# Kernel tuning notes

Hardware: AMD Instinct MI355X
Metric: run time of the kernel (lower is better)

Reference implementation:

```python
import jax, jax.numpy as jnp
import numpy as np


def setup_inputs() -> dict:
    key = jax.random.key(0)
    k1, k2 = jax.random.split(key)
    B, T, D, E = 4, 4096, 2048, 64
    x = jax.random.normal(k1, (B, T, D), dtype=jnp.float32)
    gate_w = jax.random.normal(k2, (E, D), dtype=jnp.float32) * (1.0 / np.sqrt(D))
    return {"x": x, "gate_w": gate_w, "top_k": 2}


def reference(x, gate_w, top_k):
    B, T, D = x.shape
    x_flat = x.reshape(-1, D)                      # (B*T, D)
    logits = jnp.einsum('nd,ed->ne', x_flat, gate_w)  # (B*T, E)
    weights, indices = jax.lax.top_k(logits, top_k)   # (B*T, K)
    weights = jax.nn.softmax(weights, axis=-1)
    return indices, weights
```

## Files before the change

### kernel.cpp

```cpp
#include <hip/hip_runtime.h>
#include <hip/hip_bf16.h>
#include <math.h>


constexpr int D_DIM = 2048;
constexpr int E_DIM = 64;
constexpr int BM    = 32;
constexpr int BKC   = 64;
constexpr int NCH   = D_DIM / BKC;
constexpr int LPAD  = 68;

typedef __attribute__((ext_vector_type(8))) short s16x8;
typedef __attribute__((ext_vector_type(4))) float f32x4;

static __device__ __forceinline__ short f2bf(float f) {
    __hip_bfloat16 h = __float2bfloat16(f);
    return *reinterpret_cast<short*>(&h);
}
static __device__ __forceinline__ float b2f(short s) {
    union { unsigned u; float f; } x;
    x.u = ((unsigned)(unsigned short)s) << 16;
    return x.f;
}

template <int N> static __device__ __forceinline__ void waitvm() {
    asm volatile("s_waitcnt vmcnt(%0)" :: "n"(N) : "memory");
}

__global__ __launch_bounds__(256, 1)
void pack_w(const float* __restrict__ w, short* __restrict__ wsb) {
    const int idx = blockIdx.x * 256 + threadIdx.x;
    const int e = idx >> 11, k = idx & 2047;
    const float v = w[idx];
    const short hi = f2bf(v);
    const short lo = f2bf(v - b2f(hi));
    const int g = k >> 3, j = k & 7;
    const size_t base = (size_t)g * 1024 + e * 8 + j;
    wsb[base]       = hi;
    wsb[base + 512] = lo;
}

template <bool PACKED>
__global__ __launch_bounds__(512, 4)
void router_v8(const float* __restrict__ x,
               const float* __restrict__ w,
               const short* __restrict__ wsb,
               float* __restrict__ out,
               int nrows) {
    __shared__ alignas(16) float smem[4][BM * BKC / 4 * 4];

    const int t    = threadIdx.x;
    const int lane = t & 63;
    const int wv   = t >> 6;
    const int row0 = blockIdx.x * BM;
    const int l15  = lane & 15;
    const int k8   = lane >> 4;
    const int rsel = wv & 1;
    const int e0w  = (wv >> 1) * 16;
    const int ph   = blockIdx.x & (NCH - 1);
    const char* wsb_b = (const char*)wsb;

    s16x8 Bh[4][2], Bl[4][2];

    auto loadB = [&](int p, int c) {
        const int cc = (c + ph) & (NCH - 1);
        if constexpr (PACKED) {
            #pragma unroll
            for (int s = 0; s < 2; ++s) {
                const char* bp = wsb_b + (size_t)cc * 16384
                               + (s * 4 + k8) * 2048 + (e0w + l15) * 16;
                Bh[p][s] = *reinterpret_cast<const s16x8*>(bp);
                Bl[p][s] = *reinterpret_cast<const s16x8*>(bp + 1024);
            }
        } else {
            #pragma unroll
            for (int s = 0; s < 2; ++s) {
                const float* pw = w + (size_t)(e0w + l15) * D_DIM
                                + cc * BKC + (s * 4 + k8) * 8;
                const float4 w0 = *reinterpret_cast<const float4*>(pw);
                const float4 w1 = *reinterpret_cast<const float4*>(pw + 4);
                const float wvv[8] = {w0.x, w0.y, w0.z, w0.w, w1.x, w1.y, w1.z, w1.w};
                #pragma unroll
                for (int j = 0; j < 8; ++j) {
                    const short h = f2bf(wvv[j]);
                    Bh[p][s][j] = h;
                    Bl[p][s][j] = f2bf(wvv[j] - b2f(h));
                }
            }
        }
    };

    auto stageA = [&](int p, int c) {
        const int cc = (c + ph) & (NCH - 1);
        const int r  = 4 * wv + (lane >> 4);
        const char* src = (const char*)x + (size_t)(row0 + r) * (D_DIM * 4)
                        + cc * 256 + ((l15 * 16) ^ ((r & 7) << 4));
        __builtin_amdgcn_global_load_lds(
            (const __attribute__((address_space(1))) void*)src,
            (__attribute__((address_space(3))) void*)((char*)&smem[p][0] + wv * 1024),
            16, 0, 0);
    };

    f32x4 acc;
    #pragma unroll
    for (int j = 0; j < 4; ++j) acc[j] = 0.f;

    auto compute = [&](int p) {
        const char* rp  = (const char*)&smem[p][0] + (16 * rsel + l15) * 256;
        const int   swz = ((16 * rsel + l15) & 7) << 4;
        #pragma unroll
        for (int s = 0; s < 2; ++s) {
            const int off = s * 128 + k8 * 32;
            const float4 v0 = *reinterpret_cast<const float4*>(rp + (off ^ swz));
            const float4 v1 = *reinterpret_cast<const float4*>(rp + ((off + 16) ^ swz));
            const float vv[8] = {v0.x, v0.y, v0.z, v0.w, v1.x, v1.y, v1.z, v1.w};
            s16x8 ah, al;
            #pragma unroll
            for (int j = 0; j < 8; ++j) {
                const short h = f2bf(vv[j]);
                ah[j] = h;
                al[j] = f2bf(vv[j] - b2f(h));
            }
            acc = __builtin_amdgcn_mfma_f32_16x16x32_bf16(al, Bh[p][s], acc, 0, 0, 0);
            acc = __builtin_amdgcn_mfma_f32_16x16x32_bf16(ah, Bl[p][s], acc, 0, 0, 0);
            acc = __builtin_amdgcn_mfma_f32_16x16x32_bf16(ah, Bh[p][s], acc, 0, 0, 0);
        }
    };

    #pragma unroll
    for (int p = 0; p < 4; ++p) { loadB(p, p); stageA(p, p); }

    #pragma unroll 1
    for (int cq = 0; cq < 7; ++cq) {
        #pragma unroll
        for (int p = 0; p < 4; ++p) {
            waitvm<15>();
            __builtin_amdgcn_s_barrier();
            asm volatile("" ::: "memory");
            compute(p);
            asm volatile("s_waitcnt lgkmcnt(0)" ::: "memory");
            __builtin_amdgcn_s_barrier();
            asm volatile("" ::: "memory");
            const int c = cq * 4 + p + 4;
            loadB(p, c);
            stageA(p, c);
        }
    }
    waitvm<15>(); __builtin_amdgcn_s_barrier(); asm volatile("" ::: "memory"); compute(0);
    waitvm<10>(); __builtin_amdgcn_s_barrier(); asm volatile("" ::: "memory"); compute(1);
    waitvm<5>();  __builtin_amdgcn_s_barrier(); asm volatile("" ::: "memory"); compute(2);
    waitvm<0>();  __builtin_amdgcn_s_barrier(); asm volatile("" ::: "memory"); compute(3);
    __syncthreads();

    float* lgs = &smem[0][0];
    #pragma unroll
    for (int j = 0; j < 4; ++j)
        lgs[(16 * rsel + k8 * 4 + j) * LPAD + e0w + l15] = acc[j];
    __syncthreads();

    if (wv < 4) {
        const int row = wv * 8 + (lane >> 3);
        const int seg = lane & 7;
        const float* rp = &lgs[row * LPAD + seg * 8];
        const float4 a  = *reinterpret_cast<const float4*>(rp);
        const float4 bq = *reinterpret_cast<const float4*>(rp + 4);
        const float sv[8] = {a.x, a.y, a.z, a.w, bq.x, bq.y, bq.z, bq.w};
        float m1 = sv[0]; int i1 = seg * 8;
        float m2 = -INFINITY; int i2 = 0;
        #pragma unroll
        for (int j = 1; j < 8; ++j) {
            const float v = sv[j]; const int idx = seg * 8 + j;
            if (v > m1)      { m2 = m1; i2 = i1; m1 = v; i1 = idx; }
            else if (v > m2) { m2 = v;  i2 = idx; }
        }
        #pragma unroll
        for (int d = 1; d < 8; d <<= 1) {
            const float M1 = __shfl_xor(m1, d); const int I1 = __shfl_xor(i1, d);
            const float M2 = __shfl_xor(m2, d); const int I2 = __shfl_xor(i2, d);
            const bool sw = (M1 > m1) || (M1 == m1 && I1 < i1);
            const float a1 = sw ? M1 : m1; const int j1 = sw ? I1 : i1;
            const float b1 = sw ? m1 : M1; const int kx = sw ? i1 : I1;
            const float a2 = sw ? M2 : m2; const int j2 = sw ? I2 : i2;
            const bool t2 = (b1 > a2) || (b1 == a2 && kx < j2);
            m1 = a1; i1 = j1;
            m2 = t2 ? b1 : a2; i2 = t2 ? kx : j2;
        }
        if (seg == 0) {
            const float e2v = expf(m2 - m1);
            const float sm  = 1.0f + e2v;
            const long  r   = row0 + row;
            const long  off = (long)nrows * 2;
            out[2 * r + 0]       = (float)i1;
            out[2 * r + 1]       = (float)i2;
            out[off + 2 * r + 0] = 1.0f / sm;
            out[off + 2 * r + 1] = e2v / sm;
        }
    }
}

extern "C" void kernel_launch(void* const* d_in, const int* in_sizes, int n_in,
                              void* d_out, int out_size, void* d_ws, size_t ws_size,
                              hipStream_t stream) {
    const float* x = (const float*)d_in[0];
    const float* w = (const float*)d_in[1];
    float* out = (float*)d_out;
    short* wsb = (short*)d_ws;
    const int nrows = in_sizes[0] / D_DIM;
    const int grid  = nrows / BM;
    const bool packed = ws_size >= (size_t)(E_DIM * D_DIM) * 2 * sizeof(short);

    if (packed) {
        hipLaunchKernelGGL(pack_w, dim3(E_DIM * D_DIM / 256), dim3(256), 0, stream, w, wsb);
        hipLaunchKernelGGL(router_v8<true>, dim3(grid), dim3(512), 0, stream,
                           x, w, wsb, out, nrows);
    } else {
        hipLaunchKernelGGL(router_v8<false>, dim3(grid), dim3(512), 0, stream,
                           x, w, wsb, out, nrows);
    }
}
```

Baseline: 41.05 us.

## Split K across wave groups and reuse B fragments over two M tiles

Reorganizes the eight waves into two K-halves times four expert groups, so each wave computes a 32x16 tile and reuses its loaded weight fragments across two MFMA row tiles. Partial logits from the two K halves are summed in shared memory before top-k. The packed weight layout is changed so each wave's B fragment load is contiguous per lane. Shared memory doubles, which may lower occupancy, and more A conversions happen per wave.

```diff
diff --git a/kernel.cpp b/kernel.cpp
--- a/kernel.cpp
+++ b/kernel.cpp
@@ -7,7 +7,7 @@
 constexpr int E_DIM = 64;
 constexpr int BM    = 32;
 constexpr int BKC   = 64;
-constexpr int NCH   = D_DIM / BKC;
+constexpr int NCHG  = 16;
 constexpr int LPAD  = 68;
 
 typedef __attribute__((ext_vector_type(8))) short s16x8;
@@ -35,42 +35,48 @@
     const short hi = f2bf(v);
     const short lo = f2bf(v - b2f(hi));
     const int g = k >> 3, j = k & 7;
-    const size_t base = (size_t)g * 1024 + e * 8 + j;
-    wsb[base]       = hi;
-    wsb[base + 512] = lo;
+    const int cc = g >> 3, g7 = g & 7, s = g7 >> 2, k8g = g7 & 3;
+    const int eg = e >> 4, l15e = e & 15;
+    const int Q = cc * 16 + s * 8 + eg;
+    const size_t hi16 = ((size_t)Q * 4 + k8g) * 16 + l15e;
+    const size_t lo16 = ((size_t)(Q + 4) * 4 + k8g) * 16 + l15e;
+    wsb[hi16 * 8 + j] = hi;
+    wsb[lo16 * 8 + j] = lo;
 }
 
 template <bool PACKED>
 __global__ __launch_bounds__(512, 4)
-void router_v8(const float* __restrict__ x,
-               const float* __restrict__ w,
-               const short* __restrict__ wsb,
-               float* __restrict__ out,
-               int nrows) {
-    __shared__ alignas(16) float smem[4][BM * BKC / 4 * 4];
+void router_v12(const float* __restrict__ x,
+                const float* __restrict__ w,
+                const short* __restrict__ wsb,
+                float* __restrict__ out,
+                int nrows) {
+    __shared__ alignas(16) float smem[2][4][BM * BKC];
 
     const int t    = threadIdx.x;
     const int lane = t & 63;
     const int wv   = t >> 6;
+    const int kg   = wv >> 2;
+    const int eg   = wv & 3;
     const int row0 = blockIdx.x * BM;
     const int l15  = lane & 15;
     const int k8   = lane >> 4;
-    const int rsel = wv & 1;
-    const int e0w  = (wv >> 1) * 16;
-    const int ph   = blockIdx.x & (NCH - 1);
+    const int e0w  = eg * 16;
+    const int ph   = blockIdx.x & (NCHG - 1);
     const char* wsb_b = (const char*)wsb;
 
     s16x8 Bh[4][2], Bl[4][2];
 
     auto loadB = [&](int p, int c) {
-        const int cc = (c + ph) & (NCH - 1);
+        const int cc = kg * NCHG + ((c + ph) & (NCHG - 1));
+        const size_t cb = (size_t)cc * 16384;
         if constexpr (PACKED) {
             #pragma unroll
             for (int s = 0; s < 2; ++s) {
-                const char* bp = wsb_b + (size_t)cc * 16384
-                               + (s * 4 + k8) * 2048 + (e0w + l15) * 16;
-                Bh[p][s] = *reinterpret_cast<const s16x8*>(bp);
-                Bl[p][s] = *reinterpret_cast<const s16x8*>(bp + 1024);
+                const char* hb = wsb_b + cb + (size_t)(s * 8 + 0 + eg) * 1024 + lane * 16;
+                const char* lb = wsb_b + cb + (size_t)(s * 8 + 4 + eg) * 1024 + lane * 16;
+                Bh[p][s] = *reinterpret_cast<const s16x8*>(hb);
+                Bl[p][s] = *reinterpret_cast<const s16x8*>(lb);
             }
         } else {
             #pragma unroll
@@ -91,39 +97,50 @@
     };
 
     auto stageA = [&](int p, int c) {
-        const int cc = (c + ph) & (NCH - 1);
-        const int r  = 4 * wv + (lane >> 4);
-        const char* src = (const char*)x + (size_t)(row0 + r) * (D_DIM * 4)
-                        + cc * 256 + ((l15 * 16) ^ ((r & 7) << 4));
-        __builtin_amdgcn_global_load_lds(
-            (const __attribute__((address_space(1))) void*)src,
-            (__attribute__((address_space(3))) void*)((char*)&smem[p][0] + wv * 1024),
-            16, 0, 0);
+        const int cc = kg * NCHG + ((c + ph) & (NCHG - 1));
+        #pragma unroll
+        for (int q = 0; q < 2; ++q) {
+            const int r = eg * 8 + q * 4 + (lane >> 4);
+            const char* src = (const char*)x + (size_t)(row0 + r) * (D_DIM * 4)
+                            + cc * 256 + ((l15 * 16) ^ ((r & 7) << 4));
+            __builtin_amdgcn_global_load_lds(
+                (const __attribute__((address_space(1))) void*)src,
+                (__attribute__((address_space(3))) void*)
+                    ((char*)&smem[kg][p][0] + (eg * 8 + q * 4) * 256),
+                16, 0, 0);
+        }
     };
 
-    f32x4 acc;
+    f32x4 acc[2];
     #pragma unroll
-    for (int j = 0; j < 4; ++j) acc[j] = 0.f;
+    for (int mf = 0; mf < 2; ++mf)
+        #pragma unroll
+        for (int j = 0; j < 4; ++j) acc[mf][j] = 0.f;
 
     auto compute = [&](int p) {
-        const char* rp  = (const char*)&smem[p][0] + (16 * rsel + l15) * 256;
-        const int   swz = ((16 * rsel + l15) & 7) << 4;
-        #pragma unroll
-        for (int s = 0; s < 2; ++s) {
-            const int off = s * 128 + k8 * 32;
-            const float4 v0 = *reinterpret_cast<const float4*>(rp + (off ^ swz));
-            const float4 v1 = *reinterpret_cast<const float4*>(rp + ((off + 16) ^ swz));
-            const float vv[8] = {v0.x, v0.y, v0.z, v0.w, v1.x, v1.y, v1.z, v1.w};
-            s16x8 ah, al;
+        const char* bufb = (const char*)&smem[kg][p][0];
+        #pragma unroll
+        for (int mf = 0; mf < 2; ++mf) {
+            const int r   = mf * 16 + l15;
+            const char* rp = bufb + r * 256;
+            const int swz = (r & 7) << 4;
             #pragma unroll
-            for (int j = 0; j < 8; ++j) {
-                const short h = f2bf(vv[j]);
-                ah[j] = h;
-                al[j] = f2bf(vv[j] - b2f(h));
+            for (int s = 0; s < 2; ++s) {
+                const int off = s * 128 + k8 * 32;
+                const float4 v0 = *reinterpret_cast<const float4*>(rp + (off ^ swz));
+                const float4 v1 = *reinterpret_cast<const float4*>(rp + ((off + 16) ^ swz));
+                const float vv[8] = {v0.x, v0.y, v0.z, v0.w, v1.x, v1.y, v1.z, v1.w};
+                s16x8 ah, al;
+                #pragma unroll
+                for (int j = 0; j < 8; ++j) {
+                    const short h = f2bf(vv[j]);
+                    ah[j] = h;
+                    al[j] = f2bf(vv[j] - b2f(h));
+                }
+                acc[mf] = __builtin_amdgcn_mfma_f32_16x16x32_bf16(al, Bh[p][s], acc[mf], 0, 0, 0);
+                acc[mf] = __builtin_amdgcn_mfma_f32_16x16x32_bf16(ah, Bl[p][s], acc[mf], 0, 0, 0);
+                acc[mf] = __builtin_amdgcn_mfma_f32_16x16x32_bf16(ah, Bh[p][s], acc[mf], 0, 0, 0);
             }
-            acc = __builtin_amdgcn_mfma_f32_16x16x32_bf16(al, Bh[p][s], acc, 0, 0, 0);
-            acc = __builtin_amdgcn_mfma_f32_16x16x32_bf16(ah, Bl[p][s], acc, 0, 0, 0);
-            acc = __builtin_amdgcn_mfma_f32_16x16x32_bf16(ah, Bh[p][s], acc, 0, 0, 0);
         }
     };
 
@@ -131,10 +148,10 @@
     for (int p = 0; p < 4; ++p) { loadB(p, p); stageA(p, p); }
 
     #pragma unroll 1
-    for (int cq = 0; cq < 7; ++cq) {
+    for (int cq = 0; cq < 3; ++cq) {
         #pragma unroll
         for (int p = 0; p < 4; ++p) {
-            waitvm<15>();
+            waitvm<18>();
             __builtin_amdgcn_s_barrier();
             asm volatile("" ::: "memory");
             compute(p);
@@ -146,25 +163,31 @@
             stageA(p, c);
         }
     }
-    waitvm<15>(); __builtin_amdgcn_s_barrier(); asm volatile("" ::: "memory"); compute(0);
-    waitvm<10>(); __builtin_amdgcn_s_barrier(); asm volatile("" ::: "memory"); compute(1);
-    waitvm<5>();  __builtin_amdgcn_s_barrier(); asm volatile("" ::: "memory"); compute(2);
+    waitvm<18>(); __builtin_amdgcn_s_barrier(); asm volatile("" ::: "memory"); compute(0);
+    waitvm<12>(); __builtin_amdgcn_s_barrier(); asm volatile("" ::: "memory"); compute(1);
+    waitvm<6>();  __builtin_amdgcn_s_barrier(); asm volatile("" ::: "memory"); compute(2);
     waitvm<0>();  __builtin_amdgcn_s_barrier(); asm volatile("" ::: "memory"); compute(3);
     __syncthreads();
 
-    float* lgs = &smem[0][0];
+    float* lgs = &smem[0][0][0];
     #pragma unroll
-    for (int j = 0; j < 4; ++j)
-        lgs[(16 * rsel + k8 * 4 + j) * LPAD + e0w + l15] = acc[j];
+    for (int mf = 0; mf < 2; ++mf)
+        #pragma unroll
+        for (int j = 0; j < 4; ++j)
+            lgs[((size_t)kg * BM + mf * 16 + k8 * 4 + j) * LPAD + e0w + l15] = acc[mf][j];
     __syncthreads();
 
     if (wv < 4) {
         const int row = wv * 8 + (lane >> 3);
         const int seg = lane & 7;
-        const float* rp = &lgs[row * LPAD + seg * 8];
-        const float4 a  = *reinterpret_cast<const float4*>(rp);
-        const float4 bq = *reinterpret_cast<const float4*>(rp + 4);
-        const float sv[8] = {a.x, a.y, a.z, a.w, bq.x, bq.y, bq.z, bq.w};
+        const float* r0 = &lgs[(size_t)row * LPAD + seg * 8];
+        const float* r1 = &lgs[((size_t)BM + row) * LPAD + seg * 8];
+        const float4 a0 = *reinterpret_cast<const float4*>(r0);
+        const float4 b0 = *reinterpret_cast<const float4*>(r0 + 4);
+        const float4 a1 = *reinterpret_cast<const float4*>(r1);
+        const float4 b1 = *reinterpret_cast<const float4*>(r1 + 4);
+        const float sv[8] = {a0.x + a1.x, a0.y + a1.y, a0.z + a1.z, a0.w + a1.w,
+                             b0.x + b1.x, b0.y + b1.y, b0.z + b1.z, b0.w + b1.w};
         float m1 = sv[0]; int i1 = seg * 8;
         float m2 = -INFINITY; int i2 = 0;
         #pragma unroll
@@ -178,12 +201,12 @@
             const float M1 = __shfl_xor(m1, d); const int I1 = __shfl_xor(i1, d);
             const float M2 = __shfl_xor(m2, d); const int I2 = __shfl_xor(i2, d);
             const bool sw = (M1 > m1) || (M1 == m1 && I1 < i1);
-            const float a1 = sw ? M1 : m1; const int j1 = sw ? I1 : i1;
-            const float b1 = sw ? m1 : M1; const int kx = sw ? i1 : I1;
-            const float a2 = sw ? M2 : m2; const int j2 = sw ? I2 : i2;
-            const bool t2 = (b1 > a2) || (b1 == a2 && kx < j2);
-            m1 = a1; i1 = j1;
-            m2 = t2 ? b1 : a2; i2 = t2 ? kx : j2;
+            const float a_1 = sw ? M1 : m1; const int j1 = sw ? I1 : i1;
+            const float b_1 = sw ? m1 : M1; const int kx = sw ? i1 : I1;
+            const float a_2 = sw ? M2 : m2; const int j2 = sw ? I2 : i2;
+            const bool t2 = (b_1 > a_2) || (b_1 == a_2 && kx < j2);
+            m1 = a_1; i1 = j1;
+            m2 = t2 ? b_1 : a_2; i2 = t2 ? kx : j2;
         }
         if (seg == 0) {
             const float e2v = expf(m2 - m1);
@@ -211,10 +234,10 @@
 
     if (packed) {
         hipLaunchKernelGGL(pack_w, dim3(E_DIM * D_DIM / 256), dim3(256), 0, stream, w, wsb);
-        hipLaunchKernelGGL(router_v8<true>, dim3(grid), dim3(512), 0, stream,
+        hipLaunchKernelGGL(router_v12<true>, dim3(grid), dim3(512), 0, stream,
                            x, w, wsb, out, nrows);
     } else {
-        hipLaunchKernelGGL(router_v8<false>, dim3(grid), dim3(512), 0, stream,
+        hipLaunchKernelGGL(router_v12<false>, dim3(grid), dim3(512), 0, stream,
                            x, w, wsb, out, nrows);
     }
 }
```

New measurement: 42.04 us. 2.4% more time.
